# Performance work log

Measured on AMD Instinct MI355X. Metric: run time of the kernel, lower is better.

The kernel has to match this reference:

```python
import jax, jax.numpy as jnp
import numpy as np
import math

NG, NP, NC = 300, 100000, 80
ALPHA, BETA = 0.75, 1.0
K_MAX, K_MIN = 10, 1
EPS = 1e-7


def k_schedule(epoch, total_epochs):
    t = epoch / max(1, total_epochs - 1)
    K = int(round(K_MAX - (K_MAX - K_MIN) * t))
    return max(K_MIN, min(K_MAX, K))


def setup_inputs() -> dict:
    key = jax.random.key(0)
    k1, k2, k3 = jax.random.split(key, 3)
    preds = jax.random.normal(k1, (NP, 5 + NC), dtype=jnp.float32)
    gt_boxes = jax.random.uniform(k2, (NG, 4), dtype=jnp.float32)
    gt_classes = jax.random.randint(k3, (NG,), 0, NC, dtype=jnp.int32)
    return {"preds": preds, "gt_boxes": gt_boxes, "gt_classes": gt_classes,
            "epoch": 0, "total_epochs": 300}


def _cost_matrix(preds, gt_boxes, gt_classes):
    # preds: [Np, 5+C] (xywh, obj, cls_logits); gt_boxes: [Ng, 4] xyxy
    xc, yc, w, h = preds[:, 0], preds[:, 1], preds[:, 2], preds[:, 3]
    p = jnp.stack([xc - w / 2, yc - h / 2, xc + w / 2, yc + h / 2], axis=-1)  # [Np,4] xyxy
    g = gt_boxes  # [Ng,4]

    p_ = p[None, :, :]   # [1,Np,4]
    g_ = g[:, None, :]   # [Ng,1,4]

    # IoU  (bbox_iou with ci=pred, cj=gt)
    x1 = jnp.maximum(p_[..., 0], g_[..., 0])
    y1 = jnp.maximum(p_[..., 1], g_[..., 1])
    x2 = jnp.minimum(p_[..., 2], g_[..., 2])
    y2 = jnp.minimum(p_[..., 3], g_[..., 3])
    inter = jnp.clip(x2 - x1, 0) * jnp.clip(y2 - y1, 0)          # [Ng,Np]
    area_p = jnp.clip(p[:, 2] - p[:, 0], 0) * jnp.clip(p[:, 3] - p[:, 1], 0)   # [Np]
    area_g = jnp.clip(g[:, 2] - g[:, 0], 0) * jnp.clip(g[:, 3] - g[:, 1], 0)   # [Ng]
    union = area_p[None, :] + area_g[:, None] - inter + EPS
    iou = inter / union

    # center distance
    pcx = (p[:, 0] + p[:, 2]) / 2; pcy = (p[:, 1] + p[:, 3]) / 2   # [Np]
    gcx = (g[:, 0] + g[:, 2]) / 2; gcy = (g[:, 1] + g[:, 3]) / 2   # [Ng]
    center_dist2 = (pcx[None, :] - gcx[:, None]) ** 2 + (pcy[None, :] - gcy[:, None]) ** 2

    # enclosing box diagonal
    c_w = jnp.clip(jnp.maximum(p_[..., 2], g_[..., 2]) - jnp.minimum(p_[..., 0], g_[..., 0]), EPS)
    c_h = jnp.clip(jnp.maximum(p_[..., 3], g_[..., 3]) - jnp.minimum(p_[..., 1], g_[..., 1]), EPS)
    c2 = c_w ** 2 + c_h ** 2 + EPS

    # aspect-ratio term
    wp = jnp.clip(p[:, 2] - p[:, 0], EPS); hp = jnp.clip(p[:, 3] - p[:, 1], EPS)  # [Np]
    wg = jnp.clip(g[:, 2] - g[:, 0], EPS); hg = jnp.clip(g[:, 3] - g[:, 1], EPS)  # [Ng]
    v = (4.0 / math.pi ** 2) * (jnp.arctan(wg / hg)[:, None] - jnp.arctan(wp / hp)[None, :]) ** 2
    alpha_t = jax.lax.stop_gradient(v / ((1.0 - iou) + v + EPS))   # torch.no_grad block
    ciou = iou - center_dist2 / c2 - alpha_t * v                   # [Ng,Np] (= 1 - ciou_loss)

    # classification score for each pred at its gt's class
    cls_prob = jax.nn.sigmoid(preds[:, 5:])                        # [Np,C]
    cls_score = jnp.take(cls_prob, gt_classes, axis=1).T           # [Ng,Np]

    cost = ALPHA * (1.0 - cls_score) + BETA * (1.0 - jnp.clip(ciou, 0.0, 1.0))
    return cost


def reference(preds, gt_boxes, gt_classes, epoch, total_epochs):
    Ng, Np = gt_boxes.shape[0], preds.shape[0]
    Kt = min(k_schedule(epoch, total_epochs), Np)
    cost = _cost_matrix(preds, gt_boxes, gt_classes)               # [Ng,Np]
    _, topk_idx = jax.lax.top_k(-cost, Kt)                         # [Ng,Kt] smallest cost per gt
    gt_idx = jnp.broadcast_to(jnp.arange(Ng, dtype=topk_idx.dtype)[:, None], topk_idx.shape)
    assignments = jnp.stack([topk_idx.reshape(-1), gt_idx.reshape(-1)], axis=1)  # [Ng*Kt,2]
    return cost, assignments
```

## Files before the change

### kernel.cpp

```cpp
#include <hip/hip_runtime.h>
#include <math.h>

#define NG 300
#define NP 100000
#define NC 80
#define PRED_COLS 85
#define ALPHA_C 0.75f
#define BETA_C  1.0f
#define EPS_C   1e-7f
#define TPB 256
#define NBLK ((NP + TPB - 1) / TPB)
#define BCH 10
#define CHUNK (NP / BCH)
#define KCAP 10
#define NSLAB 20
#define GSLAB (NG / NSLAB)

__device__ __forceinline__ float fast_rcp(float x) {
    return __builtin_amdgcn_rcpf(x);
}

__device__ __forceinline__ float wave_min(float v) {
#pragma unroll
    for (int off = 32; off >= 1; off >>= 1)
        v = fminf(v, __shfl_xor(v, off));
    return v;
}

__device__ __forceinline__ void wave_lexmin(float& v, int& i) {
#pragma unroll
    for (int off = 32; off >= 1; off >>= 1) {
        float ov = __shfl_xor(v, off);
        int   oi = __shfl_xor(i, off);
        if (ov < v || (ov == v && oi < i)) { v = ov; i = oi; }
    }
}

__global__ __launch_bounds__(TPB) void prep_kernel(
    const float* __restrict__ preds, float* __restrict__ probs,
    float4* __restrict__ bA, float4* __restrict__ bB)
{
    int p = blockIdx.x * TPB + threadIdx.x;
    if (p >= NP) return;
    const float* row = preds + (size_t)p * PRED_COLS;
    if (blockIdx.y == 0) {
        float xc = row[0], yc = row[1], w = row[2], h = row[3];
        float px1 = xc - w * 0.5f, py1 = yc - h * 0.5f;
        float px2 = xc + w * 0.5f, py2 = yc + h * 0.5f;
        float4 a = {px1, py1, px2, py2};
        float4 b;
        b.x = fmaxf(px2 - px1, 0.f) * fmaxf(py2 - py1, 0.f);
        b.y = (px1 + px2) * 0.5f;
        b.z = (py1 + py2) * 0.5f;
        b.w = atanf(fmaxf(px2 - px1, EPS_C) / fmaxf(py2 - py1, EPS_C));
        bA[p] = a; bB[p] = b;
#pragma unroll
        for (int c = 0; c < 40; ++c)
            probs[(size_t)c * NP + p] = fast_rcp(1.f + expf(-row[5 + c]));
    } else {
#pragma unroll
        for (int c = 40; c < 80; ++c)
            probs[(size_t)c * NP + p] = fast_rcp(1.f + expf(-row[5 + c]));
    }
}

template <bool USE_PACK>
__global__ __launch_bounds__(TPB) void cost_kernel(
    const float* __restrict__ preds, const float* __restrict__ gt_boxes,
    const int* __restrict__ gt_classes, float* __restrict__ cost,
    const float* __restrict__ probs,
    const float4* __restrict__ bA, const float4* __restrict__ bB,
    float* __restrict__ mins)
{
    __shared__ float4 sbox[GSLAB];
    __shared__ float4 smisc[GSLAB];
    __shared__ int    scls[GSLAB];
    __shared__ float  swmin[4][GSLAB];

    const int g0 = blockIdx.y * GSLAB;
    const int lane = threadIdx.x & 63;
    const int wid  = threadIdx.x >> 6;

    for (int i = threadIdx.x; i < GSLAB; i += TPB) {
        int g = g0 + i;
        float4 b = ((const float4*)gt_boxes)[g];
        float x1 = b.x, y1 = b.y, x2 = b.z, y2 = b.w;
        sbox[i] = b;
        float4 m;
        m.x = fmaxf(x2 - x1, 0.f) * fmaxf(y2 - y1, 0.f);
        m.y = (x1 + x2) * 0.5f;
        m.z = (y1 + y2) * 0.5f;
        m.w = atanf(fmaxf(x2 - x1, EPS_C) / fmaxf(y2 - y1, EPS_C));
        smisc[i] = m;
        scls[i] = USE_PACK ? gt_classes[g] * NP : gt_classes[g];
    }
    __syncthreads();

    const int p = blockIdx.x * TPB + threadIdx.x;
    const bool valid = p < NP;
    const int pc = valid ? p : NP - 1;

    float px1, py1, px2, py2, areap, pcx, pcy, atp;
    const float* row = preds + (size_t)pc * PRED_COLS;
    if (USE_PACK) {
        float4 a = bA[pc], b = bB[pc];
        px1 = a.x; py1 = a.y; px2 = a.z; py2 = a.w;
        areap = b.x; pcx = b.y; pcy = b.z; atp = b.w;
    } else {
        float xc = row[0], yc = row[1], w = row[2], h = row[3];
        px1 = xc - w * 0.5f; py1 = yc - h * 0.5f;
        px2 = xc + w * 0.5f; py2 = yc + h * 0.5f;
        areap = fmaxf(px2 - px1, 0.f) * fmaxf(py2 - py1, 0.f);
        pcx = (px1 + px2) * 0.5f; pcy = (py1 + py2) * 0.5f;
        atp = atanf(fmaxf(px2 - px1, EPS_C) / fmaxf(py2 - py1, EPS_C));
    }

    float prob[GSLAB];
#pragma unroll
    for (int i = 0; i < GSLAB; ++i) {
        if (USE_PACK) prob[i] = probs[(size_t)scls[i] + pc];
        else          prob[i] = fast_rcp(1.f + expf(-row[5 + scls[i]]));
    }

    const float VC = (float)(4.0 / (M_PI * M_PI));
    float* out = cost + (size_t)g0 * NP + p;
    float mn[GSLAB];

#pragma unroll
    for (int i = 0; i < GSLAB; ++i) {
        float4 b = sbox[i];
        float4 m = smisc[i];
        float gx1 = b.x, gy1 = b.y, gx2 = b.z, gy2 = b.w;
        float xx1 = fmaxf(px1, gx1), yy1 = fmaxf(py1, gy1);
        float xx2 = fminf(px2, gx2), yy2 = fminf(py2, gy2);
        float inter = fmaxf(xx2 - xx1, 0.f) * fmaxf(yy2 - yy1, 0.f);
        float uni = areap + m.x - inter + EPS_C;
        float iou = inter * fast_rcp(uni);
        float dx = pcx - m.y, dy = pcy - m.z;
        float cd2 = dx * dx + dy * dy;
        float cw = fmaxf(fmaxf(px2, gx2) - fminf(px1, gx1), EPS_C);
        float ch = fmaxf(fmaxf(py2, gy2) - fminf(py1, gy1), EPS_C);
        float c2 = cw * cw + ch * ch + EPS_C;
        float dat = m.w - atp;
        float v = VC * dat * dat;
        float alpha_t = v * fast_rcp(1.f - iou + v + EPS_C);
        float ciou = iou - cd2 * fast_rcp(c2) - alpha_t * v;

        float cst = ALPHA_C * (1.f - prob[i]) +
                    BETA_C * (1.f - fminf(fmaxf(ciou, 0.f), 1.f));
        mn[i] = valid ? cst : INFINITY;
        if (valid) out[(size_t)i * NP] = cst;
    }

#pragma unroll
    for (int i = 0; i < GSLAB; ++i) {
        float v = wave_min(mn[i]);
        if (lane == 0) swmin[wid][i] = v;
    }
    __syncthreads();
    if (threadIdx.x < GSLAB) {
        int t = threadIdx.x;
        float v = fminf(fminf(swmin[0][t], swmin[1][t]),
                        fminf(swmin[2][t], swmin[3][t]));
        mins[(size_t)(g0 + t) * NBLK + blockIdx.x] = v;
    }
}

__global__ __launch_bounds__(64) void thr_kernel(
    const float* __restrict__ mins, float* __restrict__ thr)
{
    int g = blockIdx.x, lane = threadIdx.x;
    const float* m = mins + (size_t)g * NBLK;
    float v[7];
#pragma unroll
    for (int j = 0; j < 7; ++j) {
        int idx = lane + j * 64;
        v[j] = (idx < NBLK) ? m[idx] : INFINITY;
    }
    float last = INFINITY;
    for (int k = 0; k < KCAP; ++k) {
        float lm = v[0];
#pragma unroll
        for (int j = 1; j < 7; ++j) lm = fminf(lm, v[j]);
        float wv = lm; int wi = lane;
        wave_lexmin(wv, wi);
        last = wv;
        if (lane == wi) {
            bool done = false;
#pragma unroll
            for (int j = 0; j < 7; ++j)
                if (!done && v[j] == lm) { v[j] = INFINITY; done = true; }
        }
    }
    if (lane == 0) thr[g] = last;
}

__global__ __launch_bounds__(TPB) void topk_partial(
    const float* __restrict__ cost, const float* __restrict__ thrbuf,
    float* __restrict__ lc, int* __restrict__ li)
{
    int g  = blockIdx.x / BCH;
    int ch = blockIdx.x % BCH;
    const float4* b4 = (const float4*)(cost + (size_t)g * NP + (size_t)ch * CHUNK);
    const int NV = CHUNK / 4;

    const int lane = threadIdx.x & 63;
    const int wid  = threadIdx.x >> 6;

    float thr = thrbuf[g];
    float ev = INFINITY;
    int   ei = 0x7fffffff;

    for (int i = threadIdx.x; i < NV; i += TPB) {
        float4 v = b4[i];
        int ib = ch * CHUNK + i * 4;
        float vmin = fminf(fminf(v.x, v.y), fminf(v.z, v.w));
        if (__ballot(vmin <= thr) == 0ull) continue;

        float vq[4] = {v.x, v.y, v.z, v.w};
#pragma unroll
        for (int q = 0; q < 4; ++q) {
            unsigned long long m = __ballot(vq[q] <= thr);
            while (m) {
                int l = __ffsll(m) - 1;
                m &= m - 1;
                float cv = __shfl(vq[q], l);
                int   ci = __shfl(ib, l) + q;
                if (!(cv <= thr)) continue;
                bool prec = (ev < cv) || (ev == cv && ei < ci);
                unsigned long long bb = __ballot(prec) & 0x3FFull;
                int pos = __popcll(bb);
                if (pos < KCAP) {
                    float pev = __shfl_up(ev, 1);
                    int   pei = __shfl_up(ei, 1);
                    if (lane > pos && lane < KCAP) { ev = pev; ei = pei; }
                    if (lane == pos)               { ev = cv;  ei = ci;  }
                    thr = fminf(thr, __shfl(ev, KCAP - 1));
                }
            }
        }
    }

    __shared__ float swv[4 * KCAP];
    __shared__ int   swi[4 * KCAP];
    if (lane < KCAP) { swv[wid * KCAP + lane] = ev; swi[wid * KCAP + lane] = ei; }
    __syncthreads();

    if (wid == 0) {
        float mv = (lane < 4 * KCAP) ? swv[lane] : INFINITY;
        int   mi = (lane < 4 * KCAP) ? swi[lane] : 0x7fffffff;
        float* oc = lc + ((size_t)g * BCH + ch) * KCAP;
        int*   oi = li + ((size_t)g * BCH + ch) * KCAP;
        for (int k = 0; k < KCAP; ++k) {
            float wv = mv; int wi = mi;
            wave_lexmin(wv, wi);
            if (lane == 0) { oc[k] = wv; oi[k] = wi; }
            if (mv == wv && mi == wi) { mv = INFINITY; mi = 0x7fffffff; }
        }
    }
}

__global__ __launch_bounds__(64) void topk_final(
    const float* __restrict__ lc, const int* __restrict__ li,
    const int* __restrict__ epoch, const int* __restrict__ total_epochs,
    float* __restrict__ out_assign)
{
    const int NE = BCH * KCAP;
    int g = blockIdx.x;
    int lane = threadIdx.x;

    float e0 = INFINITY, e1 = INFINITY;
    int   i0 = 0x7fffffff, i1 = 0x7fffffff;
    {
        const float* pc = lc + (size_t)g * NE;
        const int*   pi = li + (size_t)g * NE;
        e0 = pc[lane]; i0 = pi[lane];
        if (lane < NE - 64) { e1 = pc[lane + 64]; i1 = pi[lane + 64]; }
    }

    int ep = epoch[0], te = total_epochs[0];
    int denom = te - 1; if (denom < 1) denom = 1;
    double tt = (double)ep / (double)denom;
    int K = (int)rint(10.0 - 9.0 * tt);
    if (K < 1) K = 1; if (K > 10) K = 10;
    int Kt = (K < NP) ? K : NP;

    for (int k = 0; k < Kt; ++k) {
        bool sel0 = (e0 < e1) || (e0 == e1 && i0 < i1);
        float wv = sel0 ? e0 : e1;
        int   wi = sel0 ? i0 : i1;
        wave_lexmin(wv, wi);
        if (lane == 0) {
            out_assign[2 * ((size_t)g * Kt + k) + 0] = (float)wi;
            out_assign[2 * ((size_t)g * Kt + k) + 1] = (float)g;
        }
        if (e0 == wv && i0 == wi) { e0 = INFINITY; i0 = 0x7fffffff; }
        if (e1 == wv && i1 == wi) { e1 = INFINITY; i1 = 0x7fffffff; }
    }
}

extern "C" void kernel_launch(void* const* d_in, const int* in_sizes, int n_in,
                              void* d_out, int out_size, void* d_ws, size_t ws_size,
                              hipStream_t stream)
{
    const float* preds        = (const float*)d_in[0];
    const float* gt_boxes     = (const float*)d_in[1];
    const int*   gt_classes   = (const int*)d_in[2];
    const int*   epoch        = (const int*)d_in[3];
    const int*   total_epochs = (const int*)d_in[4];

    float* cost       = (float*)d_out;
    float* out_assign = cost + (size_t)NG * NP;

    size_t probBytes = (size_t)NC * NP * sizeof(float);
    size_t packBytes = (size_t)NP * 8 * sizeof(float);
    size_t minsBytes = (size_t)NG * NBLK * sizeof(float);
    size_t thrBytes  = 1216;
    size_t listBytes = (size_t)NG * BCH * KCAP * 8;

    char* wsp = (char*)d_ws;
    bool usePack = ws_size >= probBytes + packBytes + minsBytes + thrBytes + listBytes;

    float *probs, *minsb, *thrb, *lcb; float4 *bA, *bB; int *lib;
    if (usePack) {
        probs = (float*)wsp;
        bA    = (float4*)(wsp + probBytes);
        bB    = (float4*)(wsp + probBytes + packBytes / 2);
        minsb = (float*)(wsp + probBytes + packBytes);
        thrb  = (float*)(wsp + probBytes + packBytes + minsBytes);
        lcb   = (float*)(wsp + probBytes + packBytes + minsBytes + thrBytes);
        lib   = (int*)  (wsp + probBytes + packBytes + minsBytes + thrBytes + listBytes / 2);
    } else {
        probs = nullptr; bA = nullptr; bB = nullptr;
        minsb = (float*)wsp;
        thrb  = (float*)(wsp + minsBytes);
        lcb   = (float*)(wsp + minsBytes + thrBytes);
        lib   = (int*)  (wsp + minsBytes + thrBytes + listBytes / 2);
    }

    if (usePack) {
        prep_kernel<<<dim3(NBLK, 2), TPB, 0, stream>>>(preds, probs, bA, bB);
        cost_kernel<true ><<<dim3(NBLK, NSLAB), TPB, 0, stream>>>(
            preds, gt_boxes, gt_classes, cost, probs, bA, bB, minsb);
    } else {
        cost_kernel<false><<<dim3(NBLK, NSLAB), TPB, 0, stream>>>(
            preds, gt_boxes, gt_classes, cost, probs, bA, bB, minsb);
    }
    thr_kernel<<<NG, 64, 0, stream>>>(minsb, thrb);
    topk_partial<<<NG * BCH, TPB, 0, stream>>>(cost, thrb, lcb, lib);
    topk_final<<<NG, 64, 0, stream>>>(lcb, lib, epoch, total_epochs, out_assign);
}
```

Baseline: 245.5 us.

## Fuse top-k kernels and scan only candidate blocks using per-block minima

Merges the threshold, partial top-k and final top-k kernels into one kernel per gt row. The per-block minima are used to build a shared-memory list of blocks whose minimum is at or below the K-th smallest block minimum. Only those blocks of the cost row are then read, not the full row. This removes most of the second pass over the large cost matrix and two kernel launches. In exchange, each row is processed by a single 256-thread block with a serial candidate loop, giving only 300 blocks.

Result: faster. 221.3 us (-9.9%).

```diff
diff --git a/kernel.cpp b/kernel.cpp
--- a/kernel.cpp
+++ b/kernel.cpp
@@ -10,8 +10,6 @@
 #define EPS_C   1e-7f
 #define TPB 256
 #define NBLK ((NP + TPB - 1) / TPB)
-#define BCH 10
-#define CHUNK (NP / BCH)
 #define KCAP 10
 #define NSLAB 20
 #define GSLAB (NG / NSLAB)
@@ -166,58 +164,73 @@
     }
 }
 
-__global__ __launch_bounds__(64) void thr_kernel(
-    const float* __restrict__ mins, float* __restrict__ thr)
+__global__ __launch_bounds__(TPB) void topk_fused(
+    const float* __restrict__ cost, const float* __restrict__ mins,
+    const int* __restrict__ epoch, const int* __restrict__ total_epochs,
+    float* __restrict__ out_assign)
 {
-    int g = blockIdx.x, lane = threadIdx.x;
-    const float* m = mins + (size_t)g * NBLK;
-    float v[7];
-#pragma unroll
-    for (int j = 0; j < 7; ++j) {
-        int idx = lane + j * 64;
-        v[j] = (idx < NBLK) ? m[idx] : INFINITY;
-    }
-    float last = INFINITY;
-    for (int k = 0; k < KCAP; ++k) {
-        float lm = v[0];
-#pragma unroll
-        for (int j = 1; j < 7; ++j) lm = fminf(lm, v[j]);
-        float wv = lm; int wi = lane;
-        wave_lexmin(wv, wi);
-        last = wv;
-        if (lane == wi) {
-            bool done = false;
-#pragma unroll
-            for (int j = 0; j < 7; ++j)
-                if (!done && v[j] == lm) { v[j] = INFINITY; done = true; }
-        }
-    }
-    if (lane == 0) thr[g] = last;
-}
-
-__global__ __launch_bounds__(TPB) void topk_partial(
-    const float* __restrict__ cost, const float* __restrict__ thrbuf,
-    float* __restrict__ lc, int* __restrict__ li)
-{
-    int g  = blockIdx.x / BCH;
-    int ch = blockIdx.x % BCH;
-    const float4* b4 = (const float4*)(cost + (size_t)g * NP + (size_t)ch * CHUNK);
-    const int NV = CHUNK / 4;
-
+    const int g = blockIdx.x;
     const int lane = threadIdx.x & 63;
     const int wid  = threadIdx.x >> 6;
 
-    float thr = thrbuf[g];
-    float ev = INFINITY;
-    int   ei = 0x7fffffff;
-
-    for (int i = threadIdx.x; i < NV; i += TPB) {
-        float4 v = b4[i];
-        int ib = ch * CHUNK + i * 4;
-        float vmin = fminf(fminf(v.x, v.y), fminf(v.z, v.w));
-        if (__ballot(vmin <= thr) == 0ull) continue;
-
-        float vq[4] = {v.x, v.y, v.z, v.w};
+    __shared__ float s_thr;
+    __shared__ int   s_qn;
+    __shared__ int   qlist[NBLK];
+    __shared__ float swv[4 * KCAP];
+    __shared__ int   swi[4 * KCAP];
+
+    if (threadIdx.x == 0) s_qn = 0;
+    __syncthreads();
+
+    const float* mrow = mins + (size_t)g * NBLK;
+
+    if (wid == 0) {
+        float v[7];
+#pragma unroll
+        for (int j = 0; j < 7; ++j) {
+            int idx = lane + j * 64;
+            v[j] = (idx < NBLK) ? mrow[idx] : INFINITY;
+        }
+        float last = INFINITY;
+        for (int k = 0; k < KCAP; ++k) {
+            float lm = v[0];
+#pragma unroll
+            for (int j = 1; j < 7; ++j) lm = fminf(lm, v[j]);
+            float wv = lm; int wi = lane;
+            wave_lexmin(wv, wi);
+            last = wv;
+            if (lane == wi) {
+                bool done = false;
+#pragma unroll
+                for (int j = 0; j < 7; ++j)
+                    if (!done && v[j] == lm) { v[j] = INFINITY; done = true; }
+            }
+        }
+        if (lane == 0) s_thr = last;
+    }
+    __syncthreads();
+    const float thr0 = s_thr;
+
+    for (int b = threadIdx.x; b < NBLK; b += TPB)
+        if (mrow[b] <= thr0) qlist[atomicAdd(&s_qn, 1)] = b;
+    __syncthreads();
+    const int qn = s_qn;
+
+    float thr = thr0;
+    float ev = INFINITY; int ei = 0x7fffffff;
+
+    for (int qi = wid; qi < qn; qi += 4) {
+        const int b = qlist[qi];
+        const int ib = b * TPB + lane * 4;
+        float vq[4];
+        if (b == NBLK - 1) {
+#pragma unroll
+            for (int q = 0; q < 4; ++q)
+                vq[q] = (ib + q < NP) ? cost[(size_t)g * NP + ib + q] : INFINITY;
+        } else {
+            float4 v = *(const float4*)(cost + (size_t)g * NP + ib);
+            vq[0] = v.x; vq[1] = v.y; vq[2] = v.z; vq[3] = v.w;
+        }
 #pragma unroll
         for (int q = 0; q < 4; ++q) {
             unsigned long long m = __ballot(vq[q] <= thr);
@@ -241,61 +254,29 @@
         }
     }
 
-    __shared__ float swv[4 * KCAP];
-    __shared__ int   swi[4 * KCAP];
     if (lane < KCAP) { swv[wid * KCAP + lane] = ev; swi[wid * KCAP + lane] = ei; }
     __syncthreads();
 
     if (wid == 0) {
         float mv = (lane < 4 * KCAP) ? swv[lane] : INFINITY;
         int   mi = (lane < 4 * KCAP) ? swi[lane] : 0x7fffffff;
-        float* oc = lc + ((size_t)g * BCH + ch) * KCAP;
-        int*   oi = li + ((size_t)g * BCH + ch) * KCAP;
-        for (int k = 0; k < KCAP; ++k) {
+
+        int ep = epoch[0], te = total_epochs[0];
+        int denom = te - 1; if (denom < 1) denom = 1;
+        double tt = (double)ep / (double)denom;
+        int K = (int)rint(10.0 - 9.0 * tt);
+        if (K < 1) K = 1; if (K > 10) K = 10;
+        int Kt = (K < NP) ? K : NP;
+
+        for (int k = 0; k < Kt; ++k) {
             float wv = mv; int wi = mi;
             wave_lexmin(wv, wi);
-            if (lane == 0) { oc[k] = wv; oi[k] = wi; }
+            if (lane == 0) {
+                out_assign[2 * ((size_t)g * Kt + k) + 0] = (float)wi;
+                out_assign[2 * ((size_t)g * Kt + k) + 1] = (float)g;
+            }
             if (mv == wv && mi == wi) { mv = INFINITY; mi = 0x7fffffff; }
         }
-    }
-}
-
-__global__ __launch_bounds__(64) void topk_final(
-    const float* __restrict__ lc, const int* __restrict__ li,
-    const int* __restrict__ epoch, const int* __restrict__ total_epochs,
-    float* __restrict__ out_assign)
-{
-    const int NE = BCH * KCAP;
-    int g = blockIdx.x;
-    int lane = threadIdx.x;
-
-    float e0 = INFINITY, e1 = INFINITY;
-    int   i0 = 0x7fffffff, i1 = 0x7fffffff;
-    {
-        const float* pc = lc + (size_t)g * NE;
-        const int*   pi = li + (size_t)g * NE;
-        e0 = pc[lane]; i0 = pi[lane];
-        if (lane < NE - 64) { e1 = pc[lane + 64]; i1 = pi[lane + 64]; }
-    }
-
-    int ep = epoch[0], te = total_epochs[0];
-    int denom = te - 1; if (denom < 1) denom = 1;
-    double tt = (double)ep / (double)denom;
-    int K = (int)rint(10.0 - 9.0 * tt);
-    if (K < 1) K = 1; if (K > 10) K = 10;
-    int Kt = (K < NP) ? K : NP;
-
-    for (int k = 0; k < Kt; ++k) {
-        bool sel0 = (e0 < e1) || (e0 == e1 && i0 < i1);
-        float wv = sel0 ? e0 : e1;
-        int   wi = sel0 ? i0 : i1;
-        wave_lexmin(wv, wi);
-        if (lane == 0) {
-            out_assign[2 * ((size_t)g * Kt + k) + 0] = (float)wi;
-            out_assign[2 * ((size_t)g * Kt + k) + 1] = (float)g;
-        }
-        if (e0 == wv && i0 == wi) { e0 = INFINITY; i0 = 0x7fffffff; }
-        if (e1 == wv && i1 == wi) { e1 = INFINITY; i1 = 0x7fffffff; }
     }
 }
 
@@ -315,27 +296,19 @@
     size_t probBytes = (size_t)NC * NP * sizeof(float);
     size_t packBytes = (size_t)NP * 8 * sizeof(float);
     size_t minsBytes = (size_t)NG * NBLK * sizeof(float);
-    size_t thrBytes  = 1216;
-    size_t listBytes = (size_t)NG * BCH * KCAP * 8;
 
     char* wsp = (char*)d_ws;
-    bool usePack = ws_size >= probBytes + packBytes + minsBytes + thrBytes + listBytes;
-
-    float *probs, *minsb, *thrb, *lcb; float4 *bA, *bB; int *lib;
+    bool usePack = ws_size >= probBytes + packBytes + minsBytes;
+
+    float *probs, *minsb; float4 *bA, *bB;
     if (usePack) {
         probs = (float*)wsp;
         bA    = (float4*)(wsp + probBytes);
         bB    = (float4*)(wsp + probBytes + packBytes / 2);
         minsb = (float*)(wsp + probBytes + packBytes);
-        thrb  = (float*)(wsp + probBytes + packBytes + minsBytes);
-        lcb   = (float*)(wsp + probBytes + packBytes + minsBytes + thrBytes);
-        lib   = (int*)  (wsp + probBytes + packBytes + minsBytes + thrBytes + listBytes / 2);
     } else {
         probs = nullptr; bA = nullptr; bB = nullptr;
         minsb = (float*)wsp;
-        thrb  = (float*)(wsp + minsBytes);
-        lcb   = (float*)(wsp + minsBytes + thrBytes);
-        lib   = (int*)  (wsp + minsBytes + thrBytes + listBytes / 2);
     }
 
     if (usePack) {
@@ -346,7 +319,5 @@
         cost_kernel<false><<<dim3(NBLK, NSLAB), TPB, 0, stream>>>(
             preds, gt_boxes, gt_classes, cost, probs, bA, bB, minsb);
     }
-    thr_kernel<<<NG, 64, 0, stream>>>(minsb, thrb);
-    topk_partial<<<NG * BCH, TPB, 0, stream>>>(cost, thrb, lcb, lib);
-    topk_final<<<NG, 64, 0, stream>>>(lcb, lib, epoch, total_epochs, out_assign);
-}
+    topk_fused<<<NG, TPB, 0, stream>>>(cost, minsb, epoch, total_epochs, out_assign);
+}
```
